# Optimization experiments

Hardware: AMD Instinct MI355X
Metric: run time of the kernel (lower is better)

## Reference

```python
import jax, jax.numpy as jnp
import numpy as np

B, S, H = 4, 2048, 1024
E, K = 8, 2

def setup_inputs() -> dict:
    key = jax.random.key(0)
    ks = jax.random.split(key, 5)
    scale = 1.0 / np.sqrt(H)
    return {
        "x": jax.random.normal(ks[0], (B, S, H), dtype=jnp.float32),
        "router_w": jax.random.uniform(ks[1], (E, H), jnp.float32, -scale, scale),
        "router_b": jax.random.uniform(ks[2], (E,), jnp.float32, -scale, scale),
        "expert_w": jax.random.uniform(ks[3], (E, H, H), jnp.float32, -scale, scale),
        "expert_b": jax.random.uniform(ks[4], (E, H), jnp.float32, -scale, scale),
    }


def reference(x, router_w, router_b, expert_w, expert_b):
    # Router: [b,s,E]
    scores = jnp.einsum("bsh,eh->bse", x, router_w) + router_b
    probs = jax.nn.softmax(scores, axis=-1)
    p, expert_id = jax.lax.top_k(probs, K)          # [b,s,K]
    # Renormalize top-k probs (matches p / p.sum(dim=2))
    p = p / jnp.sum(p, axis=-1, keepdims=True)
    # Per-token combine weight per expert: [b,s,E]
    onehot = jax.nn.one_hot(expert_id, E, dtype=x.dtype)  # [b,s,K,E]
    w_comb = jnp.einsum("bske,bsk->bse", onehot, p)
    # All-expert linear (Linear: x @ W.T + b): [b,s,E,h]
    all_out = jnp.einsum("bsh,edh->bsed", x, expert_w) + expert_b
    # Weighted combine over selected experts: [b,s,h]
    return jnp.einsum("bse,bsed->bsd", w_comb, all_out)
```

## Files before the change

### kernel.cpp

```cpp
#include <hip/hip_runtime.h>
#include <hip/hip_bf16.h>
#include <math.h>

#define TOK 8192
#define HD 1024
#define NE 8
#define SLOTS 17408
#define NGRP 128

typedef _Float16 half8 __attribute__((ext_vector_type(8)));
typedef _Float16 half4v __attribute__((ext_vector_type(4)));
typedef float floatx4 __attribute__((ext_vector_type(4)));

__global__ __launch_bounds__(256) void score_cvt(
    const float* __restrict__ x,
    const float* __restrict__ rw,
    const float* __restrict__ rb,
    const float* __restrict__ ew,
    _Float16* __restrict__ xh,
    _Float16* __restrict__ wh,
    int* __restrict__ epair,
    float* __restrict__ w1out,
    int* __restrict__ hist) {
  const int tid = threadIdx.x;
  const int blk = blockIdx.x;
  if (blk >= NGRP) {
    const int g = (blk - NGRP) * 256 + tid;
    const float4* src = (const float4*)ew;
    half4v* dst = (half4v*)wh;
#pragma unroll
    for (int j = 0; j < 4; ++j) {
      float4 v = src[g + 524288 * j];
      half4v h = {(_Float16)v.x, (_Float16)v.y, (_Float16)v.z, (_Float16)v.w};
      dst[g + 524288 * j] = h;
    }
    return;
  }
  const int lane = tid & 63;
  const int wid = tid >> 6;
  __shared__ int hcnt[NE];
  if (tid < NE) hcnt[tid] = 0;
  __syncthreads();

  for (int i = 0; i < 16; ++i) {
    const int t = blk * 64 + wid * 16 + i;
    const float4* xp = (const float4*)(x + (size_t)t * HD);
    float4 xr[4];
#pragma unroll
    for (int k = 0; k < 4; ++k) xr[k] = xp[lane + 64 * k];
    _Float16* xo = xh + (size_t)t * HD;
#pragma unroll
    for (int k = 0; k < 4; ++k) {
      half4v h = {(_Float16)xr[k].x, (_Float16)xr[k].y,
                  (_Float16)xr[k].z, (_Float16)xr[k].w};
      *(half4v*)(xo + (lane + 64 * k) * 4) = h;
    }
    float sc[NE];
#pragma unroll
    for (int e = 0; e < NE; ++e) {
      const float4* wp = (const float4*)(rw + e * HD);
      float a = 0.f;
#pragma unroll
      for (int k = 0; k < 4; ++k) {
        float4 w = wp[lane + 64 * k];
        a += xr[k].x * w.x + xr[k].y * w.y + xr[k].z * w.z + xr[k].w * w.w;
      }
#pragma unroll
      for (int off = 32; off > 0; off >>= 1) a += __shfl_xor(a, off);
      sc[e] = a + rb[e];
    }
    float b1 = sc[0]; int e1 = 0;
#pragma unroll
    for (int e = 1; e < NE; ++e) if (sc[e] > b1) { b1 = sc[e]; e1 = e; }
    float b2 = -1e30f; int e2 = 0;
#pragma unroll
    for (int e = 0; e < NE; ++e) { if (e != e1 && sc[e] > b2) { b2 = sc[e]; e2 = e; } }
    if (lane == 0) {
      epair[t] = e1 | (e2 << 8);
      w1out[t] = 1.f / (1.f + expf(b2 - b1));
      atomicAdd(&hcnt[e1], 1);
      atomicAdd(&hcnt[e2], 1);
    }
  }
  __syncthreads();
  if (tid < NE) hist[tid * NGRP + blk] = hcnt[tid];
}

__global__ __launch_bounds__(256) void moe_scatter(
    const int* __restrict__ hist,
    const int* __restrict__ epair,
    const float* __restrict__ w1in,
    int* __restrict__ cntp,
    int* __restrict__ basep,
    int* __restrict__ tok_list,
    float* __restrict__ tok_w,
    int* __restrict__ slot_of) {
  const int tid = threadIdx.x;
  const int blk = blockIdx.x;
  __shared__ int pre_s[NE], tot_s[NE], alloc_s[NE];
  {
    const int e = tid >> 5;
    const int sl = tid & 31;
    int p = 0, tt = 0;
#pragma unroll
    for (int j = 0; j < 4; ++j) {
      int g = sl + 32 * j;
      int h = hist[e * NGRP + g];
      tt += h;
      p += (g < blk) ? h : 0;
    }
#pragma unroll
    for (int off = 16; off > 0; off >>= 1) {
      p += __shfl_xor(p, off);
      tt += __shfl_xor(tt, off);
    }
    if (sl == 0) { pre_s[e] = p; tot_s[e] = tt; }
  }
  __syncthreads();
  if (tid == 0) {
    int b = 0;
    for (int e = 0; e < NE; ++e) {
      alloc_s[e] = b + pre_s[e];
      if (blk == 0) { cntp[e * 64] = tot_s[e]; basep[e] = b; }
      b += (tot_s[e] + 127) & ~127;
    }
  }
  __syncthreads();
  if (tid < 64) {
    const int t = blk * 64 + tid;
    int ep = epair[t];
    int e1 = ep & 0xff, e2 = ep >> 8;
    float w1 = w1in[t];
    int s1 = atomicAdd(&alloc_s[e1], 1);
    tok_list[s1] = t; tok_w[s1] = w1; slot_of[2 * t] = s1;
    int s2 = atomicAdd(&alloc_s[e2], 1);
    tok_list[s2] = t; tok_w[s2] = 1.f - w1; slot_of[2 * t + 1] = s2;
  }
}

template <int EPI>
__global__ __launch_bounds__(256, 2) void moe_gemm(
    const _Float16* __restrict__ Ah, const _Float16* __restrict__ Bh,
    const float* __restrict__ eb,
    const int* __restrict__ cntp, const int* __restrict__ base,
    const int* __restrict__ tok_list, const float* __restrict__ tok_w,
    _Float16* __restrict__ scratch, float* __restrict__ out) {
  const int e = blockIdx.z;
  const int ce = cntp[e * 64];
  const int m0 = blockIdx.y << 7;
  if (m0 >= ce) return;
  const int sbase = base[e];
  const int n0 = blockIdx.x << 7;
  const int tid = threadIdx.x;
  const int lane = tid & 63;
  const int wid = tid >> 6;
  const int wm = wid & 1, wn = wid >> 1;

  __shared__ _Float16 A_s[128 * 128];
  __shared__ _Float16 B_s[128 * 128];
  __shared__ int tok_s[128];
  __shared__ float w_s[128];

  if (tid < 128) {
    int tk = 0; float w = 0.f;
    if (m0 + tid < ce) { tk = tok_list[sbase + m0 + tid]; w = tok_w[sbase + m0 + tid]; }
    tok_s[tid] = tk; w_s[tid] = w;
  }
  __syncthreads();

  floatx4 acc[4][4];
  floatx4 zero = {0.f, 0.f, 0.f, 0.f};
#pragma unroll
  for (int i = 0; i < 4; ++i)
#pragma unroll
    for (int j = 0; j < 4; ++j) acc[i][j] = zero;

  const int wbase = e * HD * HD;
  const int rloc = lane >> 4, sub = lane & 15;
  int agoff[8], bgoff[8];
#pragma unroll
  for (int q = 0; q < 8; ++q) {
    int row = wid * 32 + q * 4 + rloc;
    int g = sub ^ (row & 15);
    agoff[q] = tok_s[row] * HD + g * 8;
    bgoff[q] = wbase + (n0 + row) * HD + g * 8;
  }
  const int l15 = lane & 15, q4 = lane >> 4;

  for (int k0 = 0; k0 < HD; k0 += 128) {
#pragma unroll
    for (int q = 0; q < 8; ++q) {
      const int r0 = wid * 32 + q * 4;
      __builtin_amdgcn_global_load_lds(
          (const __attribute__((address_space(1))) unsigned int*)(Ah + agoff[q] + k0),
          (__attribute__((address_space(3))) unsigned int*)&A_s[r0 * 128], 16, 0, 0);
      __builtin_amdgcn_global_load_lds(
          (const __attribute__((address_space(1))) unsigned int*)(Bh + bgoff[q] + k0),
          (__attribute__((address_space(3))) unsigned int*)&B_s[r0 * 128], 16, 0, 0);
    }
    __syncthreads();
#pragma unroll
    for (int kf = 0; kf < 4; ++kf) {
      half8 afr[4], bfr[4];
      const int cc = kf * 4 + q4;
#pragma unroll
      for (int i = 0; i < 4; ++i)
        afr[i] = *(const half8*)&A_s[(wm * 64 + i * 16 + l15) * 128 + ((cc ^ l15) * 8)];
#pragma unroll
      for (int j = 0; j < 4; ++j)
        bfr[j] = *(const half8*)&B_s[(wn * 64 + j * 16 + l15) * 128 + ((cc ^ l15) * 8)];
#pragma unroll
      for (int i = 0; i < 4; ++i)
#pragma unroll
        for (int j = 0; j < 4; ++j)
          acc[i][j] = __builtin_amdgcn_mfma_f32_16x16x32_f16(afr[i], bfr[j], acc[i][j], 0, 0, 0);
    }
    __syncthreads();
  }

#pragma unroll
  for (int j = 0; j < 4; ++j) {
    int col = n0 + wn * 64 + j * 16 + l15;
    float bias = eb[e * HD + col];
#pragma unroll
    for (int i = 0; i < 4; ++i) {
      int rbase = wm * 64 + i * 16 + (q4 << 2);
#pragma unroll
      for (int r = 0; r < 4; ++r) {
        int row = rbase + r;
        float v = w_s[row] * (acc[i][j][r] + bias);
        if (EPI == 1) {
          scratch[(size_t)(sbase + m0 + row) * HD + col] = (_Float16)v;
        } else {
          if (m0 + row < ce)
            atomicAdd(&out[(size_t)tok_s[row] * HD + col], v);
        }
      }
    }
  }
}

__global__ void moe_combine(const _Float16* __restrict__ scratch,
                            const int* __restrict__ slot_of,
                            float* __restrict__ out) {
  const int tid = threadIdx.x;
  const int t = blockIdx.x * 2 + (tid >> 7);
  const int c = (tid & 127) * 8;
  int sa = slot_of[2 * t], sb = slot_of[2 * t + 1];
  half8 a = *(const half8*)&scratch[(size_t)sa * HD + c];
  half8 b = *(const half8*)&scratch[(size_t)sb * HD + c];
  float* o = out + (size_t)t * HD + c;
  float4 o0 = {(float)a[0] + (float)b[0], (float)a[1] + (float)b[1],
               (float)a[2] + (float)b[2], (float)a[3] + (float)b[3]};
  float4 o1 = {(float)a[4] + (float)b[4], (float)a[5] + (float)b[5],
               (float)a[6] + (float)b[6], (float)a[7] + (float)b[7]};
  *(float4*)o = o0;
  *(float4*)(o + 4) = o1;
}

extern "C" void kernel_launch(void* const* d_in, const int* in_sizes, int n_in,
                              void* d_out, int out_size, void* d_ws, size_t ws_size,
                              hipStream_t stream) {
  (void)in_sizes; (void)n_in;
  const float* x  = (const float*)d_in[0];
  const float* rw = (const float*)d_in[1];
  const float* rb = (const float*)d_in[2];
  const float* ew = (const float*)d_in[3];
  const float* eb = (const float*)d_in[4];
  float* out = (float*)d_out;

  char* w = (char*)d_ws;
  int*   cntp     = (int*)(w + 0);
  int*   basep    = (int*)(w + 2048);
  int*   hist     = (int*)(w + 2304);
  size_t off = 2304 + (size_t)NE * NGRP * 4;
  int*   tok_list = (int*)(w + off);  off += (size_t)SLOTS * 4;
  float* tok_w    = (float*)(w + off); off += (size_t)SLOTS * 4;
  int*   slot_of  = (int*)(w + off);  off += (size_t)TOK * 8;
  int*   epair    = (int*)(w + off);  off += (size_t)TOK * 4;
  float* w1buf    = (float*)(w + off); off += (size_t)TOK * 4;
  off = (off + 255) & ~255ull;
  size_t xh_off = off;
  size_t wh_off = xh_off + (size_t)TOK * HD * 2;
  size_t scr_off = wh_off + (size_t)NE * HD * HD * 2;
  size_t needscr = scr_off + (size_t)SLOTS * HD * 2;
  bool fastscr = ws_size >= needscr;

  if (!fastscr)
    hipMemsetAsync(d_out, 0, (size_t)out_size * sizeof(float), stream);

  _Float16* xh = (_Float16*)(w + xh_off);
  _Float16* wh = (_Float16*)(w + wh_off);
  _Float16* scr = fastscr ? (_Float16*)(w + scr_off) : nullptr;

  score_cvt<<<NGRP + 2048, 256, 0, stream>>>(x, rw, rb, ew, xh, wh,
                                             epair, w1buf, hist);
  moe_scatter<<<NGRP, 256, 0, stream>>>(hist, epair, w1buf, cntp, basep,
                                        tok_list, tok_w, slot_of);

  dim3 grid(HD / 128, TOK / 128, NE);
  if (fastscr) {
    moe_gemm<1><<<grid, 256, 0, stream>>>(xh, wh, eb, cntp, basep,
                                          tok_list, tok_w, scr, out);
    moe_combine<<<TOK / 2, 256, 0, stream>>>(scr, slot_of, out);
  } else {
    moe_gemm<0><<<grid, 256, 0, stream>>>(xh, wh, eb, cntp, basep,
                                          tok_list, tok_w, nullptr, out);
  }
}
```

Before: 197.0 us.

## Double-buffer GEMM K-tiles, remap block grid, and shrink router groups

The MoE GEMM now uses two 64-wide K stages in shared memory. The next tile's global-to-LDS load is issued before computing on the current one, so memory latency overlaps with MFMA work. The swizzle is adjusted to the narrower 64-column tiles. Block indices are remapped so neighbouring blocks share weight columns, and the router/scatter kernels use more, smaller token groups (16 tokens each, 512 groups) for more parallelism. The cost is more barriers per K step and a longer histogram prefix-sum in the scatter kernel.

After: 194.5 us. Within noise of the previous version (-1.3%).

```diff
diff --git a/kernel.cpp b/kernel.cpp
--- a/kernel.cpp
+++ b/kernel.cpp
@@ -6,7 +6,8 @@
 #define HD 1024
 #define NE 8
 #define SLOTS 17408
-#define NGRP 128
+#define NGRP 512
+#define GRPSZ 16
 
 typedef _Float16 half8 __attribute__((ext_vector_type(8)));
 typedef _Float16 half4v __attribute__((ext_vector_type(4)));
@@ -42,8 +43,9 @@
   if (tid < NE) hcnt[tid] = 0;
   __syncthreads();
 
-  for (int i = 0; i < 16; ++i) {
-    const int t = blk * 64 + wid * 16 + i;
+#pragma unroll
+  for (int i = 0; i < 4; ++i) {
+    const int t = blk * GRPSZ + wid * 4 + i;
     const float4* xp = (const float4*)(x + (size_t)t * HD);
     float4 xr[4];
 #pragma unroll
@@ -103,7 +105,7 @@
     const int sl = tid & 31;
     int p = 0, tt = 0;
 #pragma unroll
-    for (int j = 0; j < 4; ++j) {
+    for (int j = 0; j < 16; ++j) {
       int g = sl + 32 * j;
       int h = hist[e * NGRP + g];
       tt += h;
@@ -126,8 +128,8 @@
     }
   }
   __syncthreads();
-  if (tid < 64) {
-    const int t = blk * 64 + tid;
+  if (tid < GRPSZ) {
+    const int t = blk * GRPSZ + tid;
     int ep = epair[t];
     int e1 = ep & 0xff, e2 = ep >> 8;
     float w1 = w1in[t];
@@ -147,17 +149,18 @@
     _Float16* __restrict__ scratch, float* __restrict__ out) {
   const int e = blockIdx.z;
   const int ce = cntp[e * 64];
-  const int m0 = blockIdx.y << 7;
+  const int mt = ((blockIdx.y >> 3) << 3) | blockIdx.x;
+  const int m0 = mt << 7;
   if (m0 >= ce) return;
+  const int n0 = (blockIdx.y & 7) << 7;
   const int sbase = base[e];
-  const int n0 = blockIdx.x << 7;
   const int tid = threadIdx.x;
   const int lane = tid & 63;
   const int wid = tid >> 6;
   const int wm = wid & 1, wn = wid >> 1;
 
-  __shared__ _Float16 A_s[128 * 128];
-  __shared__ _Float16 B_s[128 * 128];
+  __shared__ _Float16 A_s[2][128 * 64];
+  __shared__ _Float16 B_s[2][128 * 64];
   __shared__ int tok_s[128];
   __shared__ float w_s[128];
 
@@ -176,45 +179,57 @@
     for (int j = 0; j < 4; ++j) acc[i][j] = zero;
 
   const int wbase = e * HD * HD;
-  const int rloc = lane >> 4, sub = lane & 15;
-  int agoff[8], bgoff[8];
-#pragma unroll
-  for (int q = 0; q < 8; ++q) {
-    int row = wid * 32 + q * 4 + rloc;
-    int g = sub ^ (row & 15);
+  const int rloc = lane >> 3, sub = lane & 7;
+  int agoff[4], bgoff[4];
+#pragma unroll
+  for (int q = 0; q < 4; ++q) {
+    int row = wid * 32 + q * 8 + rloc;
+    int g = sub ^ (row & 7);
     agoff[q] = tok_s[row] * HD + g * 8;
     bgoff[q] = wbase + (n0 + row) * HD + g * 8;
   }
   const int l15 = lane & 15, q4 = lane >> 4;
 
-  for (int k0 = 0; k0 < HD; k0 += 128) {
-#pragma unroll
-    for (int q = 0; q < 8; ++q) {
-      const int r0 = wid * 32 + q * 4;
+  auto stage = [&](int buf, int k0) {
+#pragma unroll
+    for (int q = 0; q < 4; ++q) {
+      const int r0 = wid * 32 + q * 8;
       __builtin_amdgcn_global_load_lds(
           (const __attribute__((address_space(1))) unsigned int*)(Ah + agoff[q] + k0),
-          (__attribute__((address_space(3))) unsigned int*)&A_s[r0 * 128], 16, 0, 0);
+          (__attribute__((address_space(3))) unsigned int*)&A_s[buf][r0 * 64], 16, 0, 0);
       __builtin_amdgcn_global_load_lds(
           (const __attribute__((address_space(1))) unsigned int*)(Bh + bgoff[q] + k0),
-          (__attribute__((address_space(3))) unsigned int*)&B_s[r0 * 128], 16, 0, 0);
-    }
-    __syncthreads();
-#pragma unroll
-    for (int kf = 0; kf < 4; ++kf) {
+          (__attribute__((address_space(3))) unsigned int*)&B_s[buf][r0 * 64], 16, 0, 0);
+    }
+  };
+
+  auto compute = [&](int buf) {
+#pragma unroll
+    for (int kf = 0; kf < 2; ++kf) {
       half8 afr[4], bfr[4];
       const int cc = kf * 4 + q4;
 #pragma unroll
       for (int i = 0; i < 4; ++i)
-        afr[i] = *(const half8*)&A_s[(wm * 64 + i * 16 + l15) * 128 + ((cc ^ l15) * 8)];
+        afr[i] = *(const half8*)&A_s[buf][(wm * 64 + i * 16 + l15) * 64 + ((cc ^ (l15 & 7)) * 8)];
 #pragma unroll
       for (int j = 0; j < 4; ++j)
-        bfr[j] = *(const half8*)&B_s[(wn * 64 + j * 16 + l15) * 128 + ((cc ^ l15) * 8)];
+        bfr[j] = *(const half8*)&B_s[buf][(wn * 64 + j * 16 + l15) * 64 + ((cc ^ (l15 & 7)) * 8)];
 #pragma unroll
       for (int i = 0; i < 4; ++i)
 #pragma unroll
         for (int j = 0; j < 4; ++j)
           acc[i][j] = __builtin_amdgcn_mfma_f32_16x16x32_f16(afr[i], bfr[j], acc[i][j], 0, 0, 0);
     }
+  };
+
+  stage(0, 0);
+  __syncthreads();
+  for (int ks = 0; ks < 16; ks += 2) {
+    stage(1, (ks + 1) * 64);
+    compute(0);
+    __syncthreads();
+    if (ks < 14) stage(0, (ks + 2) * 64);
+    compute(1);
     __syncthreads();
   }
 
```
